# Kernel optimization log

Hardware: AMD Instinct MI355X
Metric: run time of the kernel (lower is better)

The kernel has to match this reference:

```python
import jax, jax.numpy as jnp
import numpy as np

EPS = 1e-5
NEG_SLOPE = 0.01


def _bn(h, gamma, beta):
    # Training-mode batch norm over axis 0 (biased variance, like torch)
    m = h.mean(axis=0)
    v = h.var(axis=0)
    return (h - m) * jax.lax.rsqrt(v + EPS) * gamma + beta


def setup_inputs() -> dict:
    N, F, H, C = 2048, 64, 128, 2
    key = jax.random.key(0)
    ks = jax.random.split(key, 12)
    g = lambda k, shp: jax.random.normal(k, shp, dtype=jnp.float32) * 0.05
    return {
        "x": jax.random.normal(ks[0], (N, F), dtype=jnp.float32),
        "node_features": jax.random.uniform(ks[1], (N, F), dtype=jnp.float32),
        "W1": g(ks[2], (F, H)), "b1": jnp.zeros((H,), jnp.float32),
        "g1": jnp.ones((H,), jnp.float32), "be1": jnp.zeros((H,), jnp.float32),
        "W2": g(ks[3], (H, H)), "b2": jnp.zeros((H,), jnp.float32),
        "g2": jnp.ones((H,), jnp.float32), "be2": jnp.zeros((H,), jnp.float32),
        "W3": g(ks[4], (H, F)), "b3": jnp.zeros((F,), jnp.float32),
        "W5": g(ks[5], (F, H)), "b5": jnp.zeros((H,), jnp.float32),
        "g5": jnp.ones((H,), jnp.float32), "be5": jnp.zeros((H,), jnp.float32),
        "W6": g(ks[6], (H, C)), "b6": jnp.zeros((C,), jnp.float32),
    }


def reference(x, node_features, W1, b1, g1, be1, W2, b2, g2, be2, W3, b3,
              W5, b5, g5, be5, W6, b6):
    N = node_features.shape[0]
    C = W6.shape[1]
    # static upper-triangular edge list == torch.combinations(arange(N), r=2)
    ei, ej = np.triu_indices(N, k=1)

    h = node_features
    xinit = h
    h = _bn(jax.nn.leaky_relu(h @ W1 + b1, NEG_SLOPE), g1, be1)
    h = _bn(jax.nn.leaky_relu(h @ W2 + b2, NEG_SLOPE), g2, be2)
    h = h @ W3 + b3 + xinit  # [N, F]

    # edge prediction: gather pairs, elementwise mult, MLP+BN+softmax
    e = h[ei] * h[ej]  # [E, F]
    e = _bn(jax.nn.leaky_relu(e @ W5 + b5, NEG_SLOPE), g5, be5)
    edge_pred = jax.nn.softmax(e @ W6 + b6, axis=-1)  # [E, C]

    probs = jnp.zeros((N, N, C), dtype=edge_pred.dtype)
    probs = probs.at[ei, ej].set(edge_pred).at[ej, ei].set(edge_pred)
    return probs
```

## Files before the change

### kernel.cpp

```cpp
#include <hip/hip_runtime.h>
#include <hip/hip_bf16.h>


typedef short short8 __attribute__((ext_vector_type(8)));
typedef float floatx4 __attribute__((ext_vector_type(4)));

#define NN 2048
#define EPSV 1e-5f
#define EDGEF 2096128.f

__device__ __forceinline__ float bf2f(short s) {
    return __uint_as_float(((unsigned)(unsigned short)s) << 16);
}
__device__ __forceinline__ short f2bf(float f) {
    unsigned u = __float_as_uint(f);
    unsigned r = (u + 0x7FFFu + ((u >> 16) & 1u)) >> 16;
    return (short)r;
}
__device__ __forceinline__ float lrelu(float x) { return fmaxf(x, 0.01f * x); }

__device__ __forceinline__ int physB(int h, int f) {
    return ((((h >> 4) * 2 + (f >> 5)) * 64 + ((f >> 3) & 3) * 16 + (h & 15)) * 8) + (f & 7);
}

__device__ __forceinline__ void decode_tile(int bid, int& i0, int& j0, bool& str) {
    int s = bid >> 3, m = 0;
#pragma unroll 1
    while (s >= 32 - m) { s -= 32 - m; ++m; }
    i0 = ((bid & 7) + (m << 3)) * 8;
    j0 = (m + s) * 64;
    str = (s == 0);
}

__global__ __launch_bounds__(256) void k_l1(const float* __restrict__ nf,
                                            const float* __restrict__ W1,
                                            const float* __restrict__ b1,
                                            float* __restrict__ act1,
                                            float* __restrict__ stat1) {
    __shared__ float xl[8 * 64];
    __shared__ float sS[128], sQ[128];
    int t = threadIdx.x, n0 = blockIdx.x * 8;
    if (t < 128) { sS[t] = 0.f; sQ[t] = 0.f; }
    xl[t] = nf[(size_t)n0 * 64 + t];
    xl[t + 256] = nf[(size_t)n0 * 64 + t + 256];
    __syncthreads();
    int nl = t >> 5, h0 = (t & 31) * 4;
    float acc[4];
    for (int k = 0; k < 4; ++k) acc[k] = b1[h0 + k];
    for (int f = 0; f < 64; ++f) {
        float r = xl[nl * 64 + f];
        const float* wr = W1 + f * 128 + h0;
        for (int k = 0; k < 4; ++k) acc[k] = fmaf(r, wr[k], acc[k]);
    }
    for (int k = 0; k < 4; ++k) {
        float a = lrelu(acc[k]);
        act1[(size_t)(n0 + nl) * 128 + h0 + k] = a;
        atomicAdd(&sS[h0 + k], a);
        atomicAdd(&sQ[h0 + k], a * a);
    }
    __syncthreads();
    if (t < 128) atomicAdd(&stat1[t], sS[t]);
    else atomicAdd(&stat1[t], sQ[t - 128]);
}

__global__ __launch_bounds__(256) void k_l2(const float* __restrict__ act1,
                                            const float* __restrict__ stat1,
                                            const float* __restrict__ g1,
                                            const float* __restrict__ be1,
                                            const float* __restrict__ W2,
                                            const float* __restrict__ b2,
                                            float* __restrict__ act2,
                                            float* __restrict__ stat2) {
    __shared__ float a1n[8 * 128];
    __shared__ float sS[128], sQ[128];
    int t = threadIdx.x, n0 = blockIdx.x * 8;
    if (t < 128) { sS[t] = 0.f; sQ[t] = 0.f; }
    for (int k = 0; k < 4; ++k) {
        int e = t + 256 * k;
        int nl = e >> 7, h = e & 127;
        float m = stat1[h] * (1.f / 2048.f);
        float v = stat1[128 + h] * (1.f / 2048.f) - m * m;
        float sc = rsqrtf(v + EPSV);
        a1n[e] = (act1[(size_t)(n0 + nl) * 128 + h] - m) * sc * g1[h] + be1[h];
    }
    __syncthreads();
    int nl = t >> 5, h0 = (t & 31) * 4;
    float acc[4];
    for (int k = 0; k < 4; ++k) acc[k] = b2[h0 + k];
    for (int hi = 0; hi < 128; ++hi) {
        float r = a1n[nl * 128 + hi];
        const float* wr = W2 + hi * 128 + h0;
        for (int k = 0; k < 4; ++k) acc[k] = fmaf(r, wr[k], acc[k]);
    }
    for (int k = 0; k < 4; ++k) {
        float a = lrelu(acc[k]);
        act2[(size_t)(n0 + nl) * 128 + h0 + k] = a;
        atomicAdd(&sS[h0 + k], a);
        atomicAdd(&sQ[h0 + k], a * a);
    }
    __syncthreads();
    if (t < 128) atomicAdd(&stat2[t], sS[t]);
    else atomicAdd(&stat2[t], sQ[t - 128]);
}

__global__ __launch_bounds__(256) void k_l3b(const float* __restrict__ act2,
                                             const float* __restrict__ stat2,
                                             const float* __restrict__ g2,
                                             const float* __restrict__ be2,
                                             const float* __restrict__ W3,
                                             const float* __restrict__ b3,
                                             const float* __restrict__ nf,
                                             const float* __restrict__ W5,
                                             short* __restrict__ hb,
                                             short* __restrict__ T) {
    __shared__ float a2n[8 * 128];
    __shared__ short sW[8192];
    __shared__ short sH[8 * 64];
    int t = threadIdx.x, n0 = blockIdx.x * 8;
    for (int k = 0; k < 32; ++k) {
        int idx = t + 256 * k;
        sW[physB(idx & 127, idx >> 7)] = f2bf(W5[idx]);
    }
    for (int k = 0; k < 4; ++k) {
        int e = t + 256 * k;
        int nl = e >> 7, h = e & 127;
        float m = stat2[h] * (1.f / 2048.f);
        float v = stat2[128 + h] * (1.f / 2048.f) - m * m;
        float sc = rsqrtf(v + EPSV);
        a2n[e] = (act2[(size_t)(n0 + nl) * 128 + h] - m) * sc * g2[h] + be2[h];
    }
    __syncthreads();
    int nl = t >> 5, f0 = (t & 31) * 2;
    float acc[2] = {0.f, 0.f};
    for (int hi = 0; hi < 128; ++hi) {
        float r = a2n[nl * 128 + hi];
        const float* wr = W3 + hi * 64 + f0;
        acc[0] = fmaf(r, wr[0], acc[0]);
        acc[1] = fmaf(r, wr[1], acc[1]);
    }
    float v0 = acc[0] + b3[f0] + nf[(size_t)(n0 + nl) * 64 + f0];
    float v1 = acc[1] + b3[f0 + 1] + nf[(size_t)(n0 + nl) * 64 + f0 + 1];
    short s0 = f2bf(v0), s1 = f2bf(v1);
    sH[nl * 64 + f0] = s0;
    sH[nl * 64 + f0 + 1] = s1;
    unsigned p = (unsigned)(unsigned short)s0 | ((unsigned)(unsigned short)s1 << 16);
    ((unsigned*)hb)[(size_t)(n0 + nl) * 32 + (f0 >> 1)] = p;
    __syncthreads();
    for (int i = 0; i < 8; ++i) {
        for (int k = 0; k < 4; ++k) {
            int c = t + 256 * k;
            int lane = c & 63, frag = c >> 6;
            int ks = frag & 1, quad = lane >> 4;
            int fb = ks * 32 + quad * 8;
            short8 wv = ((const short8*)sW)[c];
            short8 hv = *(const short8*)(sH + i * 64 + fb);
            short8 ov;
            for (int e = 0; e < 8; ++e) ov[e] = f2bf(bf2f(wv[e]) * bf2f(hv[e]));
            ((short8*)(T + (size_t)(n0 + i) * 8192))[c] = ov;
        }
    }
}

__global__ __launch_bounds__(256) void edge_p1(
    const short* __restrict__ hb, const short* __restrict__ T,
    const float* __restrict__ b5, float* __restrict__ SQe8)
{
    int i0, j0; bool str;
    decode_tile(blockIdx.x, i0, j0, str);
    __shared__ float sS[128], sQ[128];

    int t = threadIdx.x, lane = t & 63, w = t >> 6;
    int quad = lane >> 4, col = lane & 15;
    if (t < 128) { sS[t] = 0.f; sQ[t] = 0.f; }
    __syncthreads();

    short8 hfr[4][2];
#pragma unroll
    for (int mt = 0; mt < 4; ++mt)
#pragma unroll
        for (int ks = 0; ks < 2; ++ks)
            hfr[mt][ks] = *(const short8*)(hb + (size_t)(j0 + mt * 16 + col) * 64 + ks * 32 + quad * 8);

    const short* Tb = T + (size_t)i0 * 8192;
    int toff[2][2];
#pragma unroll
    for (int n = 0; n < 2; ++n)
#pragma unroll
        for (int ks = 0; ks < 2; ++ks)
            toff[n][ks] = ((((w * 2 + n) * 2 + ks) * 64) + lane) * 8;

    float b5c[2] = { b5[w * 32 + col], b5[w * 32 + 16 + col] };
    float S[2] = {0.f, 0.f}, Q[2] = {0.f, 0.f};

    short8 ta[2][2], tb[2][2];
#pragma unroll
    for (int n = 0; n < 2; ++n)
#pragma unroll
        for (int ks = 0; ks < 2; ++ks)
            ta[n][ks] = *(const short8*)(Tb + toff[n][ks]);

    auto body1 = [&](int i, short8 (&tc)[2][2]) {
        int igi = i0 + i;
#pragma unroll
        for (int n = 0; n < 2; ++n) {
#pragma unroll
            for (int mt = 0; mt < 4; ++mt) {
                floatx4 c = {b5c[n], b5c[n], b5c[n], b5c[n]};
                c = __builtin_amdgcn_mfma_f32_16x16x32_bf16(hfr[mt][0], tc[n][0], c, 0, 0, 0);
                c = __builtin_amdgcn_mfma_f32_16x16x32_bf16(hfr[mt][1], tc[n][1], c, 0, 0, 0);
                if (!str) {
#pragma unroll
                    for (int r = 0; r < 4; ++r) {
                        float a = lrelu(c[r]);
                        S[n] += a; Q[n] = fmaf(a, a, Q[n]);
                    }
                } else {
#pragma unroll
                    for (int r = 0; r < 4; ++r) {
                        int j = j0 + mt * 16 + quad * 4 + r;
                        float a = (j > igi) ? lrelu(c[r]) : 0.f;
                        S[n] += a; Q[n] = fmaf(a, a, Q[n]);
                    }
                }
            }
        }
    };

    for (int ii = 0; ii < 8; ii += 2) {
        {
            const short* Tn = Tb + (size_t)(ii + 1) * 8192;
#pragma unroll
            for (int n = 0; n < 2; ++n)
#pragma unroll
                for (int ks = 0; ks < 2; ++ks)
                    tb[n][ks] = *(const short8*)(Tn + toff[n][ks]);
        }
        body1(ii, ta);
        if (ii + 2 < 8) {
            const short* Tn = Tb + (size_t)(ii + 2) * 8192;
#pragma unroll
            for (int n = 0; n < 2; ++n)
#pragma unroll
                for (int ks = 0; ks < 2; ++ks)
                    ta[n][ks] = *(const short8*)(Tn + toff[n][ks]);
        }
        body1(ii + 1, tb);
    }

#pragma unroll
    for (int n = 0; n < 2; ++n) {
        float s = S[n], q = Q[n];
        s += __shfl_xor(s, 16); s += __shfl_xor(s, 32);
        q += __shfl_xor(q, 16); q += __shfl_xor(q, 32);
        if (quad == 0) {
            atomicAdd(&sS[w * 32 + n * 16 + col], s);
            atomicAdd(&sQ[w * 32 + n * 16 + col], q);
        }
    }
    __syncthreads();
    float* dst = SQe8 + (blockIdx.x & 7) * 256;
    if (t < 128) atomicAdd(&dst[t], sS[t]);
    else atomicAdd(&dst[t], sQ[t - 128]);
}

__global__ __launch_bounds__(256) void edge_p2(
    const short* __restrict__ hb, const short* __restrict__ T,
    const float* __restrict__ b5, const float* __restrict__ SQe8,
    const float* __restrict__ W6, const float* __restrict__ b6,
    const float* __restrict__ g5, const float* __restrict__ be5,
    float* __restrict__ out)
{
    int i0, j0; bool str;
    decode_tile(blockIdx.x, i0, j0, str);
    __shared__ float sV[8][64];
    __shared__ float sP[8][65];
    __shared__ float sW6[128];
    __shared__ float sBB;

    int t = threadIdx.x, lane = t & 63, w = t >> 6;
    int quad = lane >> 4, col = lane & 15;

    ((float*)sV)[t] = 0.f;
    ((float*)sV)[t + 256] = 0.f;
    if (t < 128) {
        float s = 0.f, q = 0.f;
        for (int x = 0; x < 8; ++x) {
            s += SQe8[x * 256 + t];
            q += SQe8[x * 256 + 128 + t];
        }
        float m = s / EDGEF;
        float v = q / EDGEF - m * m;
        float sc = rsqrtf(v + EPSV);
        float dW = W6[2 * t] - W6[2 * t + 1];
        float sg = sc * g5[t];
        sW6[t] = sg * dW;
        ((float*)sP)[t] = (be5[t] - m * sg) * dW;
    }
    __syncthreads();
    if (w == 0) {
        float v = ((float*)sP)[lane] + ((float*)sP)[lane + 64];
        v += __shfl_xor(v, 1); v += __shfl_xor(v, 2); v += __shfl_xor(v, 4);
        v += __shfl_xor(v, 8); v += __shfl_xor(v, 16); v += __shfl_xor(v, 32);
        if (lane == 0) sBB = v + b6[0] - b6[1];
    }
    __syncthreads();
    float bb = sBB;

    float b5q[2][4], w6a[2][4], w6b[2][4];
#pragma unroll
    for (int m = 0; m < 2; ++m)
#pragma unroll
        for (int r = 0; r < 4; ++r) {
            int h = w * 32 + m * 16 + quad * 4 + r;
            b5q[m][r] = b5[h];
            float wd = sW6[h];
            w6a[m][r] = 0.505f * wd;
            w6b[m][r] = 0.495f * wd;
        }

    short8 hfr[4][2];
#pragma unroll
    for (int mt = 0; mt < 4; ++mt)
#pragma unroll
        for (int ks = 0; ks < 2; ++ks)
            hfr[mt][ks] = *(const short8*)(hb + (size_t)(j0 + mt * 16 + col) * 64 + ks * 32 + quad * 8);

    const short* Tb = T + (size_t)i0 * 8192;
    int toff[2][2];
#pragma unroll
    for (int m = 0; m < 2; ++m)
#pragma unroll
        for (int ks = 0; ks < 2; ++ks)
            toff[m][ks] = ((((w * 2 + m) * 2 + ks) * 64) + lane) * 8;

    short8 ta[2][2], tb[2][2];
#pragma unroll
    for (int m = 0; m < 2; ++m)
#pragma unroll
        for (int ks = 0; ks < 2; ++ks)
            ta[m][ks] = *(const short8*)(Tb + toff[m][ks]);

    auto body2 = [&](int i, short8 (&tc)[2][2]) {
        float dp[4] = {0.f, 0.f, 0.f, 0.f};
#pragma unroll
        for (int m = 0; m < 2; ++m) {
#pragma unroll
            for (int nj = 0; nj < 4; ++nj) {
                floatx4 c = {b5q[m][0], b5q[m][1], b5q[m][2], b5q[m][3]};
                c = __builtin_amdgcn_mfma_f32_16x16x32_bf16(tc[m][0], hfr[nj][0], c, 0, 0, 0);
                c = __builtin_amdgcn_mfma_f32_16x16x32_bf16(tc[m][1], hfr[nj][1], c, 0, 0, 0);
#pragma unroll
                for (int r = 0; r < 4; ++r) {
                    float z = c[r];
                    dp[nj] = fmaf(z, w6a[m][r], dp[nj]);
                    dp[nj] = fmaf(__builtin_fabsf(z), w6b[m][r], dp[nj]);
                }
            }
        }
#pragma unroll
        for (int nj = 0; nj < 4; ++nj) {
            float v = dp[nj];
            v += __shfl_xor(v, 16);
            v += __shfl_xor(v, 32);
            if (quad == 0) atomicAdd(&sV[i][nj * 16 + col], v);
        }
    };

    for (int ii = 0; ii < 8; ii += 2) {
        {
            const short* Tn = Tb + (size_t)(ii + 1) * 8192;
#pragma unroll
            for (int m = 0; m < 2; ++m)
#pragma unroll
                for (int ks = 0; ks < 2; ++ks)
                    tb[m][ks] = *(const short8*)(Tn + toff[m][ks]);
        }
        body2(ii, ta);
        if (ii + 2 < 8) {
            const short* Tn = Tb + (size_t)(ii + 2) * 8192;
#pragma unroll
            for (int m = 0; m < 2; ++m)
#pragma unroll
                for (int ks = 0; ks < 2; ++ks)
                    ta[m][ks] = *(const short8*)(Tn + toff[m][ks]);
        }
        body2(ii + 1, tb);
    }

    __syncthreads();
    for (int k = 0; k < 2; ++k) {
        int e = t + 256 * k;
        int il = e >> 6, jl = e & 63;
        sP[il][jl] = 1.f / (1.f + __expf(-(bb + sV[il][jl])));
    }
    __syncthreads();

    if (!str) {
        {
            int i = t >> 5, f0 = (t & 31) * 4, jl = f0 >> 1;
            float p0 = sP[i][jl], p1 = sP[i][jl + 1];
            float4 v = {p0, 1.f - p0, p1, 1.f - p1};
            *(float4*)(out + ((size_t)(i0 + i) * NN + j0) * 2 + f0) = v;
        }
        {
            int jr = t >> 2, f1 = (t & 3) * 4;
            float4 u;
#pragma unroll
            for (int e = 0; e < 4; ++e) {
                int ff = f1 + e;
                float p = sP[ff >> 1][jr];
                u[e] = (ff & 1) ? 1.f - p : p;
            }
            *(float4*)(out + ((size_t)(j0 + jr) * NN + i0) * 2 + f1) = u;
        }
    } else {
#pragma unroll
        for (int e = 0; e < 4; ++e) {
            int f = t * 4 + e;
            int i = f >> 7, jl = (f & 127) >> 1, c = f & 1;
            int ig = i0 + i, jg = j0 + jl;
            if (jg > ig) {
                float p = sP[i][jl];
                out[((size_t)ig * NN + jg) * 2 + c] = c ? 1.f - p : p;
            } else if (jg == ig) {
                out[((size_t)ig * NN + jg) * 2 + c] = 0.f;
            }
        }
#pragma unroll
        for (int e = 0; e < 4; ++e) {
            int f = t * 4 + e;
            int jr = f >> 4, ff = f & 15;
            int il = ff >> 1, c = ff & 1;
            int jg = j0 + jr, ig = i0 + il;
            if (jg > ig) {
                float p = sP[il][jr];
                out[((size_t)jg * NN + ig) * 2 + c] = c ? 1.f - p : p;
            }
        }
    }
}

extern "C" void kernel_launch(void* const* d_in, const int* in_sizes, int n_in,
                              void* d_out, int out_size, void* d_ws, size_t ws_size,
                              hipStream_t stream) {
    const float* nf  = (const float*)d_in[1];
    const float* W1  = (const float*)d_in[2];
    const float* b1  = (const float*)d_in[3];
    const float* g1  = (const float*)d_in[4];
    const float* be1 = (const float*)d_in[5];
    const float* W2  = (const float*)d_in[6];
    const float* b2  = (const float*)d_in[7];
    const float* g2  = (const float*)d_in[8];
    const float* be2 = (const float*)d_in[9];
    const float* W3  = (const float*)d_in[10];
    const float* b3  = (const float*)d_in[11];
    const float* W5  = (const float*)d_in[12];
    const float* b5  = (const float*)d_in[13];
    const float* g5  = (const float*)d_in[14];
    const float* be5 = (const float*)d_in[15];
    const float* W6  = (const float*)d_in[16];
    const float* b6  = (const float*)d_in[17];
    float* out = (float*)d_out;

    float* wsf   = (float*)d_ws;
    float* stat1 = wsf;
    float* stat2 = wsf + 256;
    float* SQe8  = wsf + 512;
    float* act1  = wsf + 4096;
    float* act2  = act1 + 262144;
    short* hb    = (short*)(act2 + 262144);
    short* Tbuf  = hb + 131072;

    hipMemsetAsync(d_ws, 0, 4096 * sizeof(float), stream);

    k_l1<<<256, 256, 0, stream>>>(nf, W1, b1, act1, stat1);
    k_l2<<<256, 256, 0, stream>>>(act1, stat1, g1, be1, W2, b2, act2, stat2);
    k_l3b<<<256, 256, 0, stream>>>(act2, stat2, g2, be2, W3, b3, nf, W5, hb, Tbuf);

    edge_p1<<<4224, 256, 0, stream>>>(hb, Tbuf, b5, SQe8);
    edge_p2<<<4224, 256, 0, stream>>>(hb, Tbuf, b5, SQe8, W6, b6, g5, be5, out);
}
```

Baseline: 267.4 us.

## Split prep kernels, hoist BN finalize, and vectorize edge stat and logit math

Moves W5 bf16 conversion into k_l1 and splits T-tensor construction into its own 2048-block kernel instead of redoing the W5 conversion in every k_l3b block. BN5 finalization moves from every edge_p2 block into a single-block k_mid kernel. edge_p1 reformulates the leaky-relu statistics as z and |z| packed sums using float2 FMAs and drops the shared-memory reduction in favour of direct global atomics. edge_p2 keeps per-row partials in registers and reduces them once into per-wave shared buffers, dropping the shared-memory atomics, and moves the forward output write into the sigmoid pass. This adds two extra kernel launches and more global atomic traffic.

```diff
diff --git a/kernel.cpp b/kernel.cpp
--- a/kernel.cpp
+++ b/kernel.cpp
@@ -4,6 +4,7 @@
 
 typedef short short8 __attribute__((ext_vector_type(8)));
 typedef float floatx4 __attribute__((ext_vector_type(4)));
+typedef float float2v __attribute__((ext_vector_type(2)));
 
 #define NN 2048
 #define EPSV 1e-5f
@@ -18,6 +19,12 @@
     return (short)r;
 }
 __device__ __forceinline__ float lrelu(float x) { return fmaxf(x, 0.01f * x); }
+__device__ __forceinline__ float2v absv(float2v x) {
+    float2v r; r.x = __builtin_fabsf(x.x); r.y = __builtin_fabsf(x.y); return r;
+}
+__device__ __forceinline__ float2v fma2(float2v a, float2v b, float2v c) {
+    float2v r; r.x = fmaf(a.x, b.x, c.x); r.y = fmaf(a.y, b.y, c.y); return r;
+}
 
 __device__ __forceinline__ int physB(int h, int f) {
     return ((((h >> 4) * 2 + (f >> 5)) * 64 + ((f >> 3) & 3) * 16 + (h & 15)) * 8) + (f & 7);
@@ -35,11 +42,17 @@
 __global__ __launch_bounds__(256) void k_l1(const float* __restrict__ nf,
                                             const float* __restrict__ W1,
                                             const float* __restrict__ b1,
+                                            const float* __restrict__ W5,
                                             float* __restrict__ act1,
-                                            float* __restrict__ stat1) {
+                                            float* __restrict__ stat1,
+                                            short* __restrict__ w5bf) {
     __shared__ float xl[8 * 64];
     __shared__ float sS[128], sQ[128];
     int t = threadIdx.x, n0 = blockIdx.x * 8;
+    if (blockIdx.x < 32) {
+        int idx = blockIdx.x * 256 + t;
+        w5bf[physB(idx & 127, idx >> 7)] = f2bf(W5[idx]);
+    }
     if (t < 128) { sS[t] = 0.f; sQ[t] = 0.f; }
     xl[t] = nf[(size_t)n0 * 64 + t];
     xl[t + 256] = nf[(size_t)n0 * 64 + t + 256];
@@ -103,24 +116,16 @@
     else atomicAdd(&stat2[t], sQ[t - 128]);
 }
 
-__global__ __launch_bounds__(256) void k_l3b(const float* __restrict__ act2,
-                                             const float* __restrict__ stat2,
-                                             const float* __restrict__ g2,
-                                             const float* __restrict__ be2,
-                                             const float* __restrict__ W3,
-                                             const float* __restrict__ b3,
-                                             const float* __restrict__ nf,
-                                             const float* __restrict__ W5,
-                                             short* __restrict__ hb,
-                                             short* __restrict__ T) {
+__global__ __launch_bounds__(256) void k_l3(const float* __restrict__ act2,
+                                            const float* __restrict__ stat2,
+                                            const float* __restrict__ g2,
+                                            const float* __restrict__ be2,
+                                            const float* __restrict__ W3,
+                                            const float* __restrict__ b3,
+                                            const float* __restrict__ nf,
+                                            short* __restrict__ hb) {
     __shared__ float a2n[8 * 128];
-    __shared__ short sW[8192];
-    __shared__ short sH[8 * 64];
     int t = threadIdx.x, n0 = blockIdx.x * 8;
-    for (int k = 0; k < 32; ++k) {
-        int idx = t + 256 * k;
-        sW[physB(idx & 127, idx >> 7)] = f2bf(W5[idx]);
-    }
     for (int k = 0; k < 4; ++k) {
         int e = t + 256 * k;
         int nl = e >> 7, h = e & 127;
@@ -140,24 +145,55 @@
     }
     float v0 = acc[0] + b3[f0] + nf[(size_t)(n0 + nl) * 64 + f0];
     float v1 = acc[1] + b3[f0 + 1] + nf[(size_t)(n0 + nl) * 64 + f0 + 1];
-    short s0 = f2bf(v0), s1 = f2bf(v1);
-    sH[nl * 64 + f0] = s0;
-    sH[nl * 64 + f0 + 1] = s1;
-    unsigned p = (unsigned)(unsigned short)s0 | ((unsigned)(unsigned short)s1 << 16);
+    unsigned p = (unsigned)(unsigned short)f2bf(v0) |
+                 ((unsigned)(unsigned short)f2bf(v1) << 16);
     ((unsigned*)hb)[(size_t)(n0 + nl) * 32 + (f0 >> 1)] = p;
-    __syncthreads();
-    for (int i = 0; i < 8; ++i) {
-        for (int k = 0; k < 4; ++k) {
-            int c = t + 256 * k;
-            int lane = c & 63, frag = c >> 6;
-            int ks = frag & 1, quad = lane >> 4;
-            int fb = ks * 32 + quad * 8;
-            short8 wv = ((const short8*)sW)[c];
-            short8 hv = *(const short8*)(sH + i * 64 + fb);
-            short8 ov;
-            for (int e = 0; e < 8; ++e) ov[e] = f2bf(bf2f(wv[e]) * bf2f(hv[e]));
-            ((short8*)(T + (size_t)(n0 + i) * 8192))[c] = ov;
-        }
+}
+
+__global__ __launch_bounds__(256) void k_bi(const short* __restrict__ w5bf,
+                                            const short* __restrict__ hb,
+                                            short* __restrict__ T) {
+    int i = blockIdx.x, t = threadIdx.x;
+    __shared__ short sHi[64];
+    if (t < 8) ((short8*)sHi)[t] = ((const short8*)(hb + (size_t)i * 64))[t];
+    __syncthreads();
+#pragma unroll
+    for (int k = 0; k < 4; ++k) {
+        int c = t + 256 * k;
+        int ks = (c >> 6) & 1, quad = (c & 63) >> 4;
+        int fb = ks * 32 + quad * 8;
+        short8 wv = ((const short8*)w5bf)[c];
+        short8 hv = *(const short8*)(sHi + fb);
+        short8 ov;
+#pragma unroll
+        for (int e = 0; e < 8; ++e) ov[e] = f2bf(bf2f(wv[e]) * bf2f(hv[e]));
+        ((short8*)(T + (size_t)i * 8192))[c] = ov;
+    }
+}
+
+__global__ void k_mid(const float* __restrict__ SQe8, const float* __restrict__ W6,
+                      const float* __restrict__ b6, const float* __restrict__ g5,
+                      const float* __restrict__ be5, float* __restrict__ w6d,
+                      float* __restrict__ b6d) {
+    __shared__ float part[128];
+    int h = threadIdx.x;
+    float s = 0.f, q = 0.f;
+    for (int x = 0; x < 8; ++x) {
+        s += SQe8[x * 256 + h];
+        q += SQe8[x * 256 + 128 + h];
+    }
+    float m = s / EDGEF;
+    float v = q / EDGEF - m * m;
+    float sc = rsqrtf(v + EPSV);
+    float dW = W6[h * 2] - W6[h * 2 + 1];
+    float sg = sc * g5[h];
+    w6d[h] = sg * dW;
+    part[h] = (be5[h] - m * sg) * dW;
+    __syncthreads();
+    if (h == 0) {
+        float acc = b6[0] - b6[1];
+        for (int k = 0; k < 128; ++k) acc += part[k];
+        b6d[0] = acc;
     }
 }
 
@@ -167,12 +203,9 @@
 {
     int i0, j0; bool str;
     decode_tile(blockIdx.x, i0, j0, str);
-    __shared__ float sS[128], sQ[128];
 
     int t = threadIdx.x, lane = t & 63, w = t >> 6;
     int quad = lane >> 4, col = lane & 15;
-    if (t < 128) { sS[t] = 0.f; sQ[t] = 0.f; }
-    __syncthreads();
 
     short8 hfr[4][2];
 #pragma unroll
@@ -190,7 +223,11 @@
             toff[n][ks] = ((((w * 2 + n) * 2 + ks) * 64) + lane) * 8;
 
     float b5c[2] = { b5[w * 32 + col], b5[w * 32 + 16 + col] };
-    float S[2] = {0.f, 0.f}, Q[2] = {0.f, 0.f};
+    float2v Sz[2], Su[2], Qzz[2], Qzu[2];
+#pragma unroll
+    for (int n = 0; n < 2; ++n) {
+        Sz[n] = 0.f; Su[n] = 0.f; Qzz[n] = 0.f; Qzu[n] = 0.f;
+    }
 
     short8 ta[2][2], tb[2][2];
 #pragma unroll
@@ -208,20 +245,24 @@
                 floatx4 c = {b5c[n], b5c[n], b5c[n], b5c[n]};
                 c = __builtin_amdgcn_mfma_f32_16x16x32_bf16(hfr[mt][0], tc[n][0], c, 0, 0, 0);
                 c = __builtin_amdgcn_mfma_f32_16x16x32_bf16(hfr[mt][1], tc[n][1], c, 0, 0, 0);
+                float2v z01, z23;
                 if (!str) {
-#pragma unroll
-                    for (int r = 0; r < 4; ++r) {
-                        float a = lrelu(c[r]);
-                        S[n] += a; Q[n] = fmaf(a, a, Q[n]);
-                    }
+                    z01.x = c[0]; z01.y = c[1];
+                    z23.x = c[2]; z23.y = c[3];
                 } else {
-#pragma unroll
-                    for (int r = 0; r < 4; ++r) {
-                        int j = j0 + mt * 16 + quad * 4 + r;
-                        float a = (j > igi) ? lrelu(c[r]) : 0.f;
-                        S[n] += a; Q[n] = fmaf(a, a, Q[n]);
-                    }
+                    int jb = j0 + mt * 16 + quad * 4;
+                    z01.x = (jb + 0 > igi) ? c[0] : 0.f;
+                    z01.y = (jb + 1 > igi) ? c[1] : 0.f;
+                    z23.x = (jb + 2 > igi) ? c[2] : 0.f;
+                    z23.y = (jb + 3 > igi) ? c[3] : 0.f;
                 }
+                float2v u01 = absv(z01), u23 = absv(z23);
+                Sz[n] += z01 + z23;
+                Su[n] += u01 + u23;
+                Qzz[n] = fma2(z01, z01, Qzz[n]);
+                Qzz[n] = fma2(z23, z23, Qzz[n]);
+                Qzu[n] = fma2(z01, u01, Qzu[n]);
+                Qzu[n] = fma2(z23, u23, Qzu[n]);
             }
         }
     };
@@ -247,75 +288,45 @@
         body1(ii + 1, tb);
     }
 
+    float* dst = SQe8 + (blockIdx.x & 7) * 256;
 #pragma unroll
     for (int n = 0; n < 2; ++n) {
-        float s = S[n], q = Q[n];
-        s += __shfl_xor(s, 16); s += __shfl_xor(s, 32);
-        q += __shfl_xor(q, 16); q += __shfl_xor(q, 32);
+        float Sa = 0.505f * (Sz[n].x + Sz[n].y) + 0.495f * (Su[n].x + Su[n].y);
+        float Qa = 0.50005f * (Qzz[n].x + Qzz[n].y) + 0.49995f * (Qzu[n].x + Qzu[n].y);
+        Sa += __shfl_xor(Sa, 16); Sa += __shfl_xor(Sa, 32);
+        Qa += __shfl_xor(Qa, 16); Qa += __shfl_xor(Qa, 32);
         if (quad == 0) {
-            atomicAdd(&sS[w * 32 + n * 16 + col], s);
-            atomicAdd(&sQ[w * 32 + n * 16 + col], q);
-        }
-    }
-    __syncthreads();
-    float* dst = SQe8 + (blockIdx.x & 7) * 256;
-    if (t < 128) atomicAdd(&dst[t], sS[t]);
-    else atomicAdd(&dst[t], sQ[t - 128]);
+            atomicAdd(&dst[w * 32 + n * 16 + col], Sa);
+            atomicAdd(&dst[128 + w * 32 + n * 16 + col], Qa);
+        }
+    }
 }
 
 __global__ __launch_bounds__(256) void edge_p2(
     const short* __restrict__ hb, const short* __restrict__ T,
-    const float* __restrict__ b5, const float* __restrict__ SQe8,
-    const float* __restrict__ W6, const float* __restrict__ b6,
-    const float* __restrict__ g5, const float* __restrict__ be5,
-    float* __restrict__ out)
+    const float* __restrict__ b5, const float* __restrict__ w6d,
+    const float* __restrict__ b6dp, float* __restrict__ out)
 {
     int i0, j0; bool str;
     decode_tile(blockIdx.x, i0, j0, str);
-    __shared__ float sV[8][64];
+    __shared__ float sV[4][8][64];
     __shared__ float sP[8][65];
-    __shared__ float sW6[128];
-    __shared__ float sBB;
 
     int t = threadIdx.x, lane = t & 63, w = t >> 6;
     int quad = lane >> 4, col = lane & 15;
 
-    ((float*)sV)[t] = 0.f;
-    ((float*)sV)[t + 256] = 0.f;
-    if (t < 128) {
-        float s = 0.f, q = 0.f;
-        for (int x = 0; x < 8; ++x) {
-            s += SQe8[x * 256 + t];
-            q += SQe8[x * 256 + 128 + t];
-        }
-        float m = s / EDGEF;
-        float v = q / EDGEF - m * m;
-        float sc = rsqrtf(v + EPSV);
-        float dW = W6[2 * t] - W6[2 * t + 1];
-        float sg = sc * g5[t];
-        sW6[t] = sg * dW;
-        ((float*)sP)[t] = (be5[t] - m * sg) * dW;
-    }
-    __syncthreads();
-    if (w == 0) {
-        float v = ((float*)sP)[lane] + ((float*)sP)[lane + 64];
-        v += __shfl_xor(v, 1); v += __shfl_xor(v, 2); v += __shfl_xor(v, 4);
-        v += __shfl_xor(v, 8); v += __shfl_xor(v, 16); v += __shfl_xor(v, 32);
-        if (lane == 0) sBB = v + b6[0] - b6[1];
-    }
-    __syncthreads();
-    float bb = sBB;
-
-    float b5q[2][4], w6a[2][4], w6b[2][4];
+    float bb = b6dp[0];
+    float b5q[2][4];
+    float2v wa2[2][2], wb2[2][2];
 #pragma unroll
     for (int m = 0; m < 2; ++m)
 #pragma unroll
         for (int r = 0; r < 4; ++r) {
             int h = w * 32 + m * 16 + quad * 4 + r;
             b5q[m][r] = b5[h];
-            float wd = sW6[h];
-            w6a[m][r] = 0.505f * wd;
-            w6b[m][r] = 0.495f * wd;
+            float wd = w6d[h];
+            ((float*)&wa2[m][r >> 1])[r & 1] = 0.505f * wd;
+            ((float*)&wb2[m][r >> 1])[r & 1] = 0.495f * wd;
         }
 
     short8 hfr[4][2];
@@ -340,8 +351,12 @@
         for (int ks = 0; ks < 2; ++ks)
             ta[m][ks] = *(const short8*)(Tb + toff[m][ks]);
 
+    float dpAll[4][8];
+
     auto body2 = [&](int i, short8 (&tc)[2][2]) {
-        float dp[4] = {0.f, 0.f, 0.f, 0.f};
+        float2v acc[4];
+#pragma unroll
+        for (int k = 0; k < 4; ++k) acc[k] = 0.f;
 #pragma unroll
         for (int m = 0; m < 2; ++m) {
 #pragma unroll
@@ -349,21 +364,18 @@
                 floatx4 c = {b5q[m][0], b5q[m][1], b5q[m][2], b5q[m][3]};
                 c = __builtin_amdgcn_mfma_f32_16x16x32_bf16(tc[m][0], hfr[nj][0], c, 0, 0, 0);
                 c = __builtin_amdgcn_mfma_f32_16x16x32_bf16(tc[m][1], hfr[nj][1], c, 0, 0, 0);
-#pragma unroll
-                for (int r = 0; r < 4; ++r) {
-                    float z = c[r];
-                    dp[nj] = fmaf(z, w6a[m][r], dp[nj]);
-                    dp[nj] = fmaf(__builtin_fabsf(z), w6b[m][r], dp[nj]);
-                }
+                float2v z01, z23;
+                z01.x = c[0]; z01.y = c[1];
+                z23.x = c[2]; z23.y = c[3];
+                float2v u01 = absv(z01), u23 = absv(z23);
+                acc[nj] = fma2(z01, wa2[m][0], acc[nj]);
+                acc[nj] = fma2(u01, wb2[m][0], acc[nj]);
+                acc[nj] = fma2(z23, wa2[m][1], acc[nj]);
+                acc[nj] = fma2(u23, wb2[m][1], acc[nj]);
             }
         }
 #pragma unroll
-        for (int nj = 0; nj < 4; ++nj) {
-            float v = dp[nj];
-            v += __shfl_xor(v, 16);
-            v += __shfl_xor(v, 32);
-            if (quad == 0) atomicAdd(&sV[i][nj * 16 + col], v);
-        }
+        for (int nj = 0; nj < 4; ++nj) dpAll[nj][i] = acc[nj].x + acc[nj].y;
     };
 
     for (int ii = 0; ii < 8; ii += 2) {
@@ -387,54 +399,57 @@
         body2(ii + 1, tb);
     }
 
-    __syncthreads();
+#pragma unroll
+    for (int i = 0; i < 8; ++i) {
+#pragma unroll
+        for (int nj = 0; nj < 4; ++nj) {
+            float v = dpAll[nj][i];
+            v += __shfl_xor(v, 16);
+            v += __shfl_xor(v, 32);
+            if (quad == (i & 3)) sV[w][i][nj * 16 + col] = v;
+        }
+    }
+    __syncthreads();
+
+#pragma unroll
     for (int k = 0; k < 2; ++k) {
         int e = t + 256 * k;
         int il = e >> 6, jl = e & 63;
-        sP[il][jl] = 1.f / (1.f + __expf(-(bb + sV[il][jl])));
+        float v = bb + sV[0][il][jl] + sV[1][il][jl] + sV[2][il][jl] + sV[3][il][jl];
+        float p = 1.f / (1.f + __expf(-v));
+        sP[il][jl] = p;
+        int ig = i0 + il, jg = j0 + jl;
+        float2v pr;
+        if (!str || jg > ig) {
+            pr.x = p; pr.y = 1.f - p;
+            *(float2v*)(out + ((size_t)ig * NN + jg) * 2) = pr;
+        } else if (jg == ig) {
+            pr.x = 0.f; pr.y = 0.f;
+            *(float2v*)(out + ((size_t)ig * NN + jg) * 2) = pr;
+        }
     }
     __syncthreads();
 
     if (!str) {
-        {
-            int i = t >> 5, f0 = (t & 31) * 4, jl = f0 >> 1;
-            float p0 = sP[i][jl], p1 = sP[i][jl + 1];
-            float4 v = {p0, 1.f - p0, p1, 1.f - p1};
-            *(float4*)(out + ((size_t)(i0 + i) * NN + j0) * 2 + f0) = v;
-        }
-        {
-            int jr = t >> 2, f1 = (t & 3) * 4;
-            float4 u;
-#pragma unroll
-            for (int e = 0; e < 4; ++e) {
-                int ff = f1 + e;
-                float p = sP[ff >> 1][jr];
-                u[e] = (ff & 1) ? 1.f - p : p;
-            }
-            *(float4*)(out + ((size_t)(j0 + jr) * NN + i0) * 2 + f1) = u;
-        }
+        int jr = t >> 2, f1 = (t & 3) * 4;
+        float4 u;
+#pragma unroll
+        for (int e = 0; e < 4; ++e) {
+            int ff = f1 + e;
+            float p = sP[ff >> 1][jr];
+            ((float*)&u)[e] = (ff & 1) ? 1.f - p : p;
+        }
+        *(float4*)(out + ((size_t)(j0 + jr) * NN + i0) * 2 + f1) = u;
     } else {
-#pragma unroll
-        for (int e = 0; e < 4; ++e) {
-            int f = t * 4 + e;
-            int i = f >> 7, jl = (f & 127) >> 1, c = f & 1;
-            int ig = i0 + i, jg = j0 + jl;
-            if (jg > ig) {
-                float p = sP[i][jl];
-                out[((size_t)ig * NN + jg) * 2 + c] = c ? 1.f - p : p;
-            } else if (jg == ig) {
-                out[((size_t)ig * NN + jg) * 2 + c] = 0.f;
-            }
-        }
 #pragma unroll
         for (int e = 0; e < 4; ++e) {
             int f = t * 4 + e;
             int jr = f >> 4, ff = f & 15;
-            int il = ff >> 1, c = ff & 1;
+            int il = ff >> 1, c2 = ff & 1;
             int jg = j0 + jr, ig = i0 + il;
             if (jg > ig) {
                 float p = sP[il][jr];
-                out[((size_t)jg * NN + ig) * 2 + c] = c ? 1.f - p : p;
+                out[((size_t)jg * NN + ig) * 2 + c2] = c2 ? 1.f - p : p;
             }
         }
     }
@@ -466,17 +481,22 @@
     float* stat1 = wsf;
     float* stat2 = wsf + 256;
     float* SQe8  = wsf + 512;
+    float* w6d   = wsf + 2560;
+    float* b6dp  = wsf + 2688;
     float* act1  = wsf + 4096;
     float* act2  = act1 + 262144;
     short* hb    = (short*)(act2 + 262144);
-    short* Tbuf  = hb + 131072;
+    short* w5bf  = hb + 131072;
+    short* Tbuf  = w5bf + 8192;
 
     hipMemsetAsync(d_ws, 0, 4096 * sizeof(float), stream);
 
-    k_l1<<<256, 256, 0, stream>>>(nf, W1, b1, act1, stat1);
+    k_l1<<<256, 256, 0, stream>>>(nf, W1, b1, W5, act1, stat1, w5bf);
     k_l2<<<256, 256, 0, stream>>>(act1, stat1, g1, be1, W2, b2, act2, stat2);
-    k_l3b<<<256, 256, 0, stream>>>(act2, stat2, g2, be2, W3, b3, nf, W5, hb, Tbuf);
+    k_l3<<<256, 256, 0, stream>>>(act2, stat2, g2, be2, W3, b3, nf, hb);
+    k_bi<<<2048, 256, 0, stream>>>(w5bf, hb, Tbuf);
 
     edge_p1<<<4224, 256, 0, stream>>>(hb, Tbuf, b5, SQe8);
-    edge_p2<<<4224, 256, 0, stream>>>(hb, Tbuf, b5, SQe8, W6, b6, g5, be5, out);
-}
+    k_mid<<<1, 128, 0, stream>>>(SQe8, W6, b6, g5, be5, w6d, b6dp);
+    edge_p2<<<4224, 256, 0, stream>>>(hb, Tbuf, b5, w6d, b6dp, out);
+}
```

Measured after the change: 396.8 us. 1.48x slower.
